# Kernel tuning notes

Measured on AMD Instinct MI355X. Metric: run time of the kernel, lower is better.

The kernel has to match this reference:

```python
import jax, jax.numpy as jnp
import numpy as np

N_NODES = 50000
N_EDGES = 800000
IN_C = 16
HID_C = 16
OUT_C = 10
N_GRAPHS = 500
EDGE_DIM = 3
MLP_HID = 25
BN_EPS = 1e-5


def setup_inputs() -> dict:
    key = jax.random.key(0)
    ks = iter(jax.random.split(key, 40))

    def nrm(shape, scale=1.0):
        return jax.random.normal(next(ks), shape, dtype=jnp.float32) * scale

    inp = {}
    inp["x"] = nrm((N_NODES, IN_C))
    inp["edge_index"] = jax.random.randint(next(ks), (2, N_EDGES), 0, N_NODES, dtype=jnp.int32)
    inp["edge_attr"] = jax.random.uniform(next(ks), (N_EDGES, EDGE_DIM), dtype=jnp.float32)
    inp["batch"] = jnp.sort(jax.random.randint(next(ks), (N_NODES,), 0, N_GRAPHS, dtype=jnp.int32))

    def bn_params():
        g = jax.random.uniform(next(ks), (MLP_HID,), minval=0.8, maxval=1.2, dtype=jnp.float32)
        b = nrm((MLP_HID,), 0.1)
        mu = nrm((MLP_HID,), 0.1)
        var = jax.random.uniform(next(ks), (MLP_HID,), minval=0.5, maxval=1.5, dtype=jnp.float32)
        return g, b, mu, var

    # edge MLP 1: 3 -> 25 -> IN_C*HID_C
    inp["W1a"] = nrm((EDGE_DIM, MLP_HID), 0.3)
    inp["b1a"] = nrm((MLP_HID,), 0.05)
    inp["g1"], inp["bt1"], inp["m1"], inp["v1"] = bn_params()
    inp["W1b"] = nrm((MLP_HID, IN_C * HID_C), 0.1)
    inp["b1b"] = nrm((IN_C * HID_C,), 0.05)
    inp["root1"] = nrm((IN_C, HID_C), 0.2)
    inp["bias1"] = nrm((HID_C,), 0.05)

    # edge MLP 2: 3 -> 25 -> HID_C*HID_C
    inp["W2a"] = nrm((EDGE_DIM, MLP_HID), 0.3)
    inp["b2a"] = nrm((MLP_HID,), 0.05)
    inp["g2"], inp["bt2"], inp["m2"], inp["v2"] = bn_params()
    inp["W2b"] = nrm((MLP_HID, HID_C * HID_C), 0.1)
    inp["b2b"] = nrm((HID_C * HID_C,), 0.05)
    inp["root2"] = nrm((HID_C, HID_C), 0.2)
    inp["bias2"] = nrm((HID_C,), 0.05)

    # final MLP([HID_C, OUT_C]) -> single plain linear (plain_last)
    inp["fcW"] = nrm((HID_C, OUT_C), 0.2)
    inp["fcb"] = nrm((OUT_C,), 0.05)
    return inp


def _edge_mlp(e, Wa, ba, g, bt, mu, var, Wb, bb):
    # Linear -> BatchNorm(eval) -> ReLU -> (dropout=eval identity) -> Linear
    h = e @ Wa + ba
    h = g * (h - mu) * jax.lax.rsqrt(var + BN_EPS) + bt
    h = jax.nn.relu(h)
    return h @ Wb + bb


def _nnconv(x, src, dst, w_edge, root, bias, out_dim):
    # message: x_j [E,in] times per-edge weight [E,in,out]
    msg = jnp.einsum("ei,eio->eo", x[src], w_edge)
    agg = jax.ops.segment_sum(msg, dst, num_segments=N_NODES)
    deg = jax.ops.segment_sum(jnp.ones((src.shape[0],), msg.dtype), dst, num_segments=N_NODES)
    agg = agg / jnp.maximum(deg, 1.0)[:, None]  # mean aggregation
    return agg + x @ root + bias


def reference(x, edge_index, edge_attr, batch,
              W1a, b1a, g1, bt1, m1, v1, W1b, b1b, root1, bias1,
              W2a, b2a, g2, bt2, m2, v2, W2b, b2b, root2, bias2,
              fcW, fcb):
    src, dst = edge_index[0], edge_index[1]

    w1 = _edge_mlp(edge_attr, W1a, b1a, g1, bt1, m1, v1, W1b, b1b).reshape(-1, IN_C, HID_C)
    x = jax.nn.elu(_nnconv(x, src, dst, w1, root1, bias1, HID_C))

    w2 = _edge_mlp(edge_attr, W2a, b2a, g2, bt2, m2, v2, W2b, b2b).reshape(-1, HID_C, HID_C)
    x = jax.nn.elu(_nnconv(x, src, dst, w2, root2, bias2, HID_C))

    # global mean pooling over graphs
    pooled = jax.ops.segment_sum(x, batch, num_segments=N_GRAPHS)
    cnt = jax.ops.segment_sum(jnp.ones((x.shape[0],), x.dtype), batch, num_segments=N_GRAPHS)
    pooled = pooled / jnp.maximum(cnt, 1.0)[:, None]

    return pooled @ fcW + fcb  # [N_GRAPHS, OUT_C]
```

## Files before the change

kernel.cpp:

```cpp
#include <hip/hip_runtime.h>
#include <math.h>

#define N_NODES 50000
#define N_EDGES 800000
#define IN_C 16
#define HID_C 16
#define OUT_C 10
#define N_GRAPHS 500
#define EDGE_DIM 3
#define MLP_HID 25
#define BN_EPS 1e-5f

#define SCAN_NB ((N_NODES + 255) / 256)

typedef __attribute__((ext_vector_type(8))) short short8;
typedef __attribute__((ext_vector_type(4))) float f32x4;
typedef __attribute__((ext_vector_type(2))) float f32x2;
union U4S8 { uint4 u; short8 s; };


__global__ __launch_bounds__(256) void prep_graph_kernel(
    const float* __restrict__ W1a, const float* __restrict__ b1a,
    const float* __restrict__ g1, const float* __restrict__ bt1,
    const float* __restrict__ m1, const float* __restrict__ v1,
    const float* __restrict__ W2a, const float* __restrict__ b2a,
    const float* __restrict__ g2, const float* __restrict__ bt2,
    const float* __restrict__ m2, const float* __restrict__ v2,
    const int* __restrict__ batch,
    float* __restrict__ AC1, float* __restrict__ AC2,
    int* __restrict__ goff)
{
    int t = threadIdx.x;
    if (blockIdx.x == 0) {
        if (t < 26) {
            int k = t;
            if (k < 25) {
                float sc = g1[k] / sqrtf(v1[k] + BN_EPS);
                AC1[k*4+0] = sc * W1a[0*MLP_HID+k];
                AC1[k*4+1] = sc * W1a[1*MLP_HID+k];
                AC1[k*4+2] = sc * W1a[2*MLP_HID+k];
                AC1[k*4+3] = sc * (b1a[k] - m1[k]) + bt1[k];
            } else {
                AC1[100] = 0.f; AC1[101] = 0.f; AC1[102] = 0.f; AC1[103] = 1.f;
            }
        } else if (t >= 32 && t < 58) {
            int k = t - 32;
            if (k < 25) {
                float sc = g2[k] / sqrtf(v2[k] + BN_EPS);
                AC2[k*4+0] = sc * W2a[0*MLP_HID+k];
                AC2[k*4+1] = sc * W2a[1*MLP_HID+k];
                AC2[k*4+2] = sc * W2a[2*MLP_HID+k];
                AC2[k*4+3] = sc * (b2a[k] - m2[k]) + bt2[k];
            } else {
                AC2[100] = 0.f; AC2[101] = 0.f; AC2[102] = 0.f; AC2[103] = 1.f;
            }
        }
    }
    int g = blockIdx.x * blockDim.x + t;
    if (g <= N_GRAPHS) {
        int lo = 0, hi = N_NODES;
        while (lo < hi) {
            int mid = (lo + hi) >> 1;
            if (batch[mid] < g) lo = mid + 1; else hi = mid;
        }
        goff[g] = lo;
    }
}

__global__ __launch_bounds__(256) void pack_w_kernel(
    const float* __restrict__ W1b, const float* __restrict__ b1b,
    const float* __restrict__ W2b, const float* __restrict__ b2b,
    unsigned int* __restrict__ WHI1, unsigned int* __restrict__ WHI2)
{
    int t = blockIdx.x * 256 + threadIdx.x;
    if (t >= 1664) return;
    const float *Wb, *bb; unsigned int *WH;
    int tl = t;
    if (t < 832) { Wb = W1b; bb = b1b; WH = WHI1; }
    else { tl = t - 832; Wb = W2b; bb = b2b; WH = WHI2; }
    int m = tl >> 6;
    int L = tl & 63;
    int q = L >> 4, o = L & 15;
    unsigned int hi[8];
    for (int j = 0; j < 8; ++j) {
        int kp = m*32 + q*8 + j;
        int k = kp >> 4, i = kp & 15;
        float w = (k < 25) ? Wb[k*256 + i*16 + o] : bb[i*16 + o];
        unsigned int u = __float_as_uint(w);
        hi[j] = (u + 0x7FFFu + ((u >> 16) & 1u)) >> 16;
    }
    int base = (m*64 + L) * 4;
    for (int d = 0; d < 4; ++d)
        WH[base + d] = hi[2*d] | (hi[2*d+1] << 16);
}


__global__ __launch_bounds__(256) void rank_kernel(const int* __restrict__ dst,
                                                   int* __restrict__ cnt,
                                                   int* __restrict__ rank) {
    int e = blockIdx.x * blockDim.x + threadIdx.x;
    if (e < N_EDGES) rank[e] = atomicAdd(&cnt[dst[e]], 1);
}

__global__ __launch_bounds__(256) void scan_p1(const int* __restrict__ cnt,
                                               int* __restrict__ bsum) {
    __shared__ int lds[256];
    int t = threadIdx.x;
    int idx = blockIdx.x * 256 + t;
    lds[t] = (idx < N_NODES) ? cnt[idx] : 0;
    __syncthreads();
    for (int d = 128; d > 0; d >>= 1) {
        if (t < d) lds[t] += lds[t + d];
        __syncthreads();
    }
    if (t == 0) bsum[blockIdx.x] = lds[0];
}

__global__ __launch_bounds__(256) void scan_p2(const int* __restrict__ bsum,
                                               int* __restrict__ bpre,
                                               int* __restrict__ off) {
    __shared__ int lds[256];
    int t = threadIdx.x;
    lds[t] = (t < SCAN_NB) ? bsum[t] : 0;
    __syncthreads();
    for (int d = 1; d < 256; d <<= 1) {
        int v = (t >= d) ? lds[t - d] : 0;
        __syncthreads();
        lds[t] += v;
        __syncthreads();
    }
    if (t < SCAN_NB) bpre[t] = (t > 0) ? lds[t - 1] : 0;
    if (t == 255) off[N_NODES] = lds[255];
}

__global__ __launch_bounds__(256) void scan_p3(const int* __restrict__ cnt,
                                               const int* __restrict__ bpre,
                                               int* __restrict__ off) {
    __shared__ int lds[256];
    int t = threadIdx.x;
    int idx = blockIdx.x * 256 + t;
    int v = (idx < N_NODES) ? cnt[idx] : 0;
    lds[t] = v;
    __syncthreads();
    for (int d = 1; d < 256; d <<= 1) {
        int u = (t >= d) ? lds[t - d] : 0;
        __syncthreads();
        lds[t] += u;
        __syncthreads();
    }
    if (idx < N_NODES) off[idx] = bpre[blockIdx.x] + lds[t] - v;
}

__global__ __launch_bounds__(256) void pos2_kernel(const int* __restrict__ dst,
                                                   const int* __restrict__ off,
                                                   int* __restrict__ rank) {
    int e = blockIdx.x * blockDim.x + threadIdx.x;
    if (e < N_EDGES) rank[e] = off[dst[e]] + rank[e];
}


__device__ __forceinline__ U4S8 packH(float h, float4 xl, float4 xh) {
    f32x2 h2; h2.x = h; h2.y = h;
    f32x2 m0; m0.x = xl.x; m0.y = xl.y; m0 *= h2;
    f32x2 m1; m1.x = xl.z; m1.y = xl.w; m1 *= h2;
    f32x2 m2; m2.x = xh.x; m2.y = xh.y; m2 *= h2;
    f32x2 m3; m3.x = xh.z; m3.y = xh.w; m3 *= h2;
    U4S8 r;
    r.u.x = __builtin_amdgcn_perm(__float_as_uint(m0.y), __float_as_uint(m0.x), 0x07060302u);
    r.u.y = __builtin_amdgcn_perm(__float_as_uint(m1.y), __float_as_uint(m1.x), 0x07060302u);
    r.u.z = __builtin_amdgcn_perm(__float_as_uint(m2.y), __float_as_uint(m2.x), 0x07060302u);
    r.u.w = __builtin_amdgcn_perm(__float_as_uint(m3.y), __float_as_uint(m3.x), 0x07060302u);
    return r;
}

__global__ __launch_bounds__(256) void edge_mfma3_kernel(
    const float* __restrict__ xin,
    const int* __restrict__ src,
    const int* __restrict__ P,
    const float* __restrict__ eattr,
    const float* __restrict__ AC,
    const unsigned int* __restrict__ WHI,
    float* __restrict__ msg_buf)
{
    const int tid  = threadIdx.x;
    const int wave = tid >> 6;
    const int lane = tid & 63;
    const int q    = lane >> 4;
    const int el   = lane & 15;
    const int i0   = (q & 1) * 8;
    const int b    = q >> 1;
    const int e0   = (blockIdx.x * 4 + wave) * 16;
    const int e    = e0 + el;

    const int s = src[e];
    const float a0 = eattr[(size_t)e*3+0];
    const float a1 = eattr[(size_t)e*3+1];
    const float a2 = eattr[(size_t)e*3+2];
    const uint4 pp = *(const uint4*)(P + e0 + q*4);
    const float4* xp = (const float4*)(xin + (size_t)s*16 + i0);
    const float4 xl = xp[0], xh = xp[1];

    f32x4 acc = {0.f, 0.f, 0.f, 0.f};
    #pragma unroll 1
    for (int m = 0; m < 13; ++m) {
        const float4 Ak = *(const float4*)(AC + (2*m + b)*4);
        U4S8 w; w.u = ((const uint4*)WHI)[m*64 + lane];
        float h = fmaxf(fmaf(a2, Ak.z, fmaf(a1, Ak.y, fmaf(a0, Ak.x, Ak.w))), 0.f);
        U4S8 hf = packH(h, xl, xh);
        acc = __builtin_amdgcn_mfma_f32_16x16x32_bf16(hf.s, w.s, acc, 0, 0, 0);
    }

    msg_buf[(size_t)((unsigned)pp.x) * HID_C + el] = acc[0];
    msg_buf[(size_t)((unsigned)pp.y) * HID_C + el] = acc[1];
    msg_buf[(size_t)((unsigned)pp.z) * HID_C + el] = acc[2];
    msg_buf[(size_t)((unsigned)pp.w) * HID_C + el] = acc[3];
}

__global__ __launch_bounds__(256) void node_gather_kernel(
    const float* __restrict__ xin, const float* __restrict__ msg_buf,
    const int* __restrict__ off,
    const float* __restrict__ root, const float* __restrict__ bias,
    float* __restrict__ xout)
{
    int t = blockIdx.x * blockDim.x + threadIdx.x;
    int n = t >> 4;
    int o = t & 15;
    if (n >= N_NODES) return;
    int lo = off[n], hi = off[n+1];
    float inv = 1.f / fmaxf((float)(hi - lo), 1.f);

    float s0 = 0.f, s1 = 0.f, s2 = 0.f, s3 = 0.f;
    int r = lo;
    for (; r + 4 <= hi; r += 4) {
        s0 += msg_buf[(size_t)r     * HID_C + o];
        s1 += msg_buf[(size_t)(r+1) * HID_C + o];
        s2 += msg_buf[(size_t)(r+2) * HID_C + o];
        s3 += msg_buf[(size_t)(r+3) * HID_C + o];
    }
    for (; r < hi; ++r) s0 += msg_buf[(size_t)r * HID_C + o];
    float s = (s0 + s1) + (s2 + s3);

    float acc = fmaf(s, inv, bias[o]);
    const float* xr = xin + (size_t)n * IN_C;
    #pragma unroll
    for (int i = 0; i < IN_C; ++i)
        acc = fmaf(xr[i], root[i*HID_C+o], acc);
    xout[(size_t)n*HID_C + o] = acc > 0.f ? acc : (expf(acc) - 1.f);
}

__global__ __launch_bounds__(64) void pool_final_kernel(
    const float* __restrict__ xin, const int* __restrict__ goff,
    const float* __restrict__ fcW, const float* __restrict__ fcb,
    float* __restrict__ out)
{
    __shared__ float part[4][HID_C];
    __shared__ float pooled[HID_C];
    int g = blockIdx.x;
    int t = threadIdx.x;
    int c = t & 15, sub = t >> 4;
    int lo = goff[g], hi = goff[g+1];
    float s = 0.f;
    for (int n = lo + sub; n < hi; n += 4)
        s += xin[(size_t)n*HID_C + c];
    part[sub][c] = s;
    __syncthreads();
    if (t < HID_C) {
        pooled[t] = (part[0][t] + part[1][t] + part[2][t] + part[3][t])
                    / fmaxf((float)(hi - lo), 1.f);
    }
    __syncthreads();
    if (t < OUT_C) {
        float acc = fcb[t];
        #pragma unroll
        for (int i = 0; i < HID_C; ++i)
            acc = fmaf(pooled[i], fcW[i*OUT_C+t], acc);
        out[g*OUT_C + t] = acc;
    }
}


extern "C" void kernel_launch(void* const* d_in, const int* in_sizes, int n_in,
                              void* d_out, int out_size, void* d_ws, size_t ws_size,
                              hipStream_t stream)
{
    const float* x     = (const float*)d_in[0];
    const int*   ei    = (const int*)d_in[1];
    const float* eattr = (const float*)d_in[2];
    const int*   batch = (const int*)d_in[3];
    const float* W1a   = (const float*)d_in[4];
    const float* b1a   = (const float*)d_in[5];
    const float* g1    = (const float*)d_in[6];
    const float* bt1   = (const float*)d_in[7];
    const float* m1    = (const float*)d_in[8];
    const float* v1    = (const float*)d_in[9];
    const float* W1b   = (const float*)d_in[10];
    const float* b1b   = (const float*)d_in[11];
    const float* root1 = (const float*)d_in[12];
    const float* bias1 = (const float*)d_in[13];
    const float* W2a   = (const float*)d_in[14];
    const float* b2a   = (const float*)d_in[15];
    const float* g2    = (const float*)d_in[16];
    const float* bt2   = (const float*)d_in[17];
    const float* m2    = (const float*)d_in[18];
    const float* v2    = (const float*)d_in[19];
    const float* W2b   = (const float*)d_in[20];
    const float* b2b   = (const float*)d_in[21];
    const float* root2 = (const float*)d_in[22];
    const float* bias2 = (const float*)d_in[23];
    const float* fcW   = (const float*)d_in[24];
    const float* fcb   = (const float*)d_in[25];

    const int* src = ei;
    const int* dst = ei + N_EDGES;

    float* ws   = (float*)d_ws;
    float* MSG  = ws;
    float* X1   = ws + 12800000;
    float* X2   = ws + 13600000;
    int*   RANK = (int*)(ws + 14400000);
    int*   CNT  = (int*)(ws + 15200000);
    int*   OFF  = (int*)(ws + 15250000);
    int*   GOFF = (int*)(ws + 15300064);
    unsigned int* WHI1 = (unsigned int*)(ws + 15300576);
    unsigned int* WHI2 = (unsigned int*)(ws + 15303904);
    float* AC1  = ws + 15307232;
    float* AC2  = ws + 15307344;
    int*   BSUM = (int*)(ws + 15307456);
    int*   BPRE = (int*)(ws + 15307712);

    hipMemsetAsync(CNT, 0, N_NODES * sizeof(int), stream);
    prep_graph_kernel<<<3, 256, 0, stream>>>(W1a, b1a, g1, bt1, m1, v1,
                                             W2a, b2a, g2, bt2, m2, v2,
                                             batch, AC1, AC2, GOFF);
    pack_w_kernel<<<7, 256, 0, stream>>>(W1b, b1b, W2b, b2b, WHI1, WHI2);
    rank_kernel<<<N_EDGES/256, 256, 0, stream>>>(dst, CNT, RANK);
    scan_p1<<<SCAN_NB, 256, 0, stream>>>(CNT, BSUM);
    scan_p2<<<1, 256, 0, stream>>>(BSUM, BPRE, OFF);
    scan_p3<<<SCAN_NB, 256, 0, stream>>>(CNT, BPRE, OFF);
    pos2_kernel<<<N_EDGES/256, 256, 0, stream>>>(dst, OFF, RANK);

    edge_mfma3_kernel<<<N_EDGES/64, 256, 0, stream>>>(x, src, RANK, eattr,
                                                      AC1, WHI1, MSG);
    node_gather_kernel<<<(N_NODES*16+255)/256, 256, 0, stream>>>(x, MSG, OFF,
                                                                 root1, bias1, X1);

    edge_mfma3_kernel<<<N_EDGES/64, 256, 0, stream>>>(X1, src, RANK, eattr,
                                                      AC2, WHI2, MSG);
    node_gather_kernel<<<(N_NODES*16+255)/256, 256, 0, stream>>>(X1, MSG, OFF,
                                                                 root2, bias2, X2);

    pool_final_kernel<<<N_GRAPHS, 64, 0, stream>>>(X2, GOFF, fcW, fcb, (float*)d_out);
}
```

Measured before the change: 310.4 us.

## Process two 16-edge tiles per wave in edge MFMA kernel and merge setup kernels

The edge kernel now has each wave handle 32 edges as two independent 16-edge MFMA chains. The per-iteration weight fragment and AC coefficient loads are shared across both chains, and the grid is halved. The two small setup kernels (weight packing and BN folding/graph offsets) are merged into one launch to save a kernel launch. Each lane now computes both even and odd hidden activations and selects one, which adds some VALU work and register pressure in exchange for reuse and more instruction-level parallelism.

```diff
diff --git a/kernel.cpp b/kernel.cpp
--- a/kernel.cpp
+++ b/kernel.cpp
@@ -19,21 +19,48 @@
 union U4S8 { uint4 u; short8 s; };
 
 
-__global__ __launch_bounds__(256) void prep_graph_kernel(
+__global__ __launch_bounds__(256) void setup_kernel(
     const float* __restrict__ W1a, const float* __restrict__ b1a,
     const float* __restrict__ g1, const float* __restrict__ bt1,
     const float* __restrict__ m1, const float* __restrict__ v1,
     const float* __restrict__ W2a, const float* __restrict__ b2a,
     const float* __restrict__ g2, const float* __restrict__ bt2,
     const float* __restrict__ m2, const float* __restrict__ v2,
+    const float* __restrict__ W1b, const float* __restrict__ b1b,
+    const float* __restrict__ W2b, const float* __restrict__ b2b,
     const int* __restrict__ batch,
     float* __restrict__ AC1, float* __restrict__ AC2,
+    unsigned int* __restrict__ WHI1, unsigned int* __restrict__ WHI2,
     int* __restrict__ goff)
 {
-    int t = threadIdx.x;
-    if (blockIdx.x == 0) {
-        if (t < 26) {
-            int k = t;
+    const int blk = blockIdx.x;
+    const int tid = threadIdx.x;
+    if (blk < 7) {
+        int t = blk * 256 + tid;
+        if (t >= 1664) return;
+        const float *Wb, *bb; unsigned int *WH;
+        int tl = t;
+        if (t < 832) { Wb = W1b; bb = b1b; WH = WHI1; }
+        else { tl = t - 832; Wb = W2b; bb = b2b; WH = WHI2; }
+        int m = tl >> 6;
+        int L = tl & 63;
+        int q = L >> 4, o = L & 15;
+        unsigned int hi[8];
+        for (int j = 0; j < 8; ++j) {
+            int kp = m*32 + q*8 + j;
+            int k = kp >> 4, i = kp & 15;
+            float w = (k < 25) ? Wb[k*256 + i*16 + o] : bb[i*16 + o];
+            unsigned int u = __float_as_uint(w);
+            hi[j] = (u + 0x7FFFu + ((u >> 16) & 1u)) >> 16;
+        }
+        int base = (m*64 + L) * 4;
+        for (int d = 0; d < 4; ++d)
+            WH[base + d] = hi[2*d] | (hi[2*d+1] << 16);
+        return;
+    }
+    if (blk == 7) {
+        if (tid < 26) {
+            int k = tid;
             if (k < 25) {
                 float sc = g1[k] / sqrtf(v1[k] + BN_EPS);
                 AC1[k*4+0] = sc * W1a[0*MLP_HID+k];
@@ -43,8 +70,8 @@
             } else {
                 AC1[100] = 0.f; AC1[101] = 0.f; AC1[102] = 0.f; AC1[103] = 1.f;
             }
-        } else if (t >= 32 && t < 58) {
-            int k = t - 32;
+        } else if (tid >= 32 && tid < 58) {
+            int k = tid - 32;
             if (k < 25) {
                 float sc = g2[k] / sqrtf(v2[k] + BN_EPS);
                 AC2[k*4+0] = sc * W2a[0*MLP_HID+k];
@@ -56,7 +83,7 @@
             }
         }
     }
-    int g = blockIdx.x * blockDim.x + t;
+    int g = (blk - 7) * 256 + tid;
     if (g <= N_GRAPHS) {
         int lo = 0, hi = N_NODES;
         while (lo < hi) {
@@ -65,33 +92,6 @@
         }
         goff[g] = lo;
     }
-}
-
-__global__ __launch_bounds__(256) void pack_w_kernel(
-    const float* __restrict__ W1b, const float* __restrict__ b1b,
-    const float* __restrict__ W2b, const float* __restrict__ b2b,
-    unsigned int* __restrict__ WHI1, unsigned int* __restrict__ WHI2)
-{
-    int t = blockIdx.x * 256 + threadIdx.x;
-    if (t >= 1664) return;
-    const float *Wb, *bb; unsigned int *WH;
-    int tl = t;
-    if (t < 832) { Wb = W1b; bb = b1b; WH = WHI1; }
-    else { tl = t - 832; Wb = W2b; bb = b2b; WH = WHI2; }
-    int m = tl >> 6;
-    int L = tl & 63;
-    int q = L >> 4, o = L & 15;
-    unsigned int hi[8];
-    for (int j = 0; j < 8; ++j) {
-        int kp = m*32 + q*8 + j;
-        int k = kp >> 4, i = kp & 15;
-        float w = (k < 25) ? Wb[k*256 + i*16 + o] : bb[i*16 + o];
-        unsigned int u = __float_as_uint(w);
-        hi[j] = (u + 0x7FFFu + ((u >> 16) & 1u)) >> 16;
-    }
-    int base = (m*64 + L) * 4;
-    for (int d = 0; d < 4; ++d)
-        WH[base + d] = hi[2*d] | (hi[2*d+1] << 16);
 }
 
 
@@ -173,7 +173,7 @@
     return r;
 }
 
-__global__ __launch_bounds__(256) void edge_mfma3_kernel(
+__global__ __launch_bounds__(256) void edge_mfma4_kernel(
     const float* __restrict__ xin,
     const int* __restrict__ src,
     const int* __restrict__ P,
@@ -188,32 +188,52 @@
     const int q    = lane >> 4;
     const int el   = lane & 15;
     const int i0   = (q & 1) * 8;
-    const int b    = q >> 1;
-    const int e0   = (blockIdx.x * 4 + wave) * 16;
-    const int e    = e0 + el;
-
-    const int s = src[e];
-    const float a0 = eattr[(size_t)e*3+0];
-    const float a1 = eattr[(size_t)e*3+1];
-    const float a2 = eattr[(size_t)e*3+2];
-    const uint4 pp = *(const uint4*)(P + e0 + q*4);
-    const float4* xp = (const float4*)(xin + (size_t)s*16 + i0);
-    const float4 xl = xp[0], xh = xp[1];
-
-    f32x4 acc = {0.f, 0.f, 0.f, 0.f};
+    const bool bsel = (q >> 1) != 0;
+    const int E0   = (blockIdx.x * 4 + wave) * 32;
+    const int eA   = E0 + el;
+    const int eB   = E0 + 16 + el;
+
+    const int sA = src[eA], sB = src[eB];
+    const float aA0 = eattr[(size_t)eA*3+0];
+    const float aA1 = eattr[(size_t)eA*3+1];
+    const float aA2 = eattr[(size_t)eA*3+2];
+    const float aB0 = eattr[(size_t)eB*3+0];
+    const float aB1 = eattr[(size_t)eB*3+1];
+    const float aB2 = eattr[(size_t)eB*3+2];
+    const uint4 ppA = *(const uint4*)(P + E0 + q*4);
+    const uint4 ppB = *(const uint4*)(P + E0 + 16 + q*4);
+    const float4* xpA = (const float4*)(xin + (size_t)sA*16 + i0);
+    const float4 xlA = xpA[0], xhA = xpA[1];
+    const float4* xpB = (const float4*)(xin + (size_t)sB*16 + i0);
+    const float4 xlB = xpB[0], xhB = xpB[1];
+
+    f32x4 accA = {0.f, 0.f, 0.f, 0.f};
+    f32x4 accB = {0.f, 0.f, 0.f, 0.f};
     #pragma unroll 1
     for (int m = 0; m < 13; ++m) {
-        const float4 Ak = *(const float4*)(AC + (2*m + b)*4);
+        const float4 Ae = *(const float4*)(AC + m*8);
+        const float4 Ao = *(const float4*)(AC + m*8 + 4);
         U4S8 w; w.u = ((const uint4*)WHI)[m*64 + lane];
-        float h = fmaxf(fmaf(a2, Ak.z, fmaf(a1, Ak.y, fmaf(a0, Ak.x, Ak.w))), 0.f);
-        U4S8 hf = packH(h, xl, xh);
-        acc = __builtin_amdgcn_mfma_f32_16x16x32_bf16(hf.s, w.s, acc, 0, 0, 0);
-    }
-
-    msg_buf[(size_t)((unsigned)pp.x) * HID_C + el] = acc[0];
-    msg_buf[(size_t)((unsigned)pp.y) * HID_C + el] = acc[1];
-    msg_buf[(size_t)((unsigned)pp.z) * HID_C + el] = acc[2];
-    msg_buf[(size_t)((unsigned)pp.w) * HID_C + el] = acc[3];
+        float hAe = fmaxf(fmaf(aA2, Ae.z, fmaf(aA1, Ae.y, fmaf(aA0, Ae.x, Ae.w))), 0.f);
+        float hAo = fmaxf(fmaf(aA2, Ao.z, fmaf(aA1, Ao.y, fmaf(aA0, Ao.x, Ao.w))), 0.f);
+        float hA  = bsel ? hAo : hAe;
+        float hBe = fmaxf(fmaf(aB2, Ae.z, fmaf(aB1, Ae.y, fmaf(aB0, Ae.x, Ae.w))), 0.f);
+        float hBo = fmaxf(fmaf(aB2, Ao.z, fmaf(aB1, Ao.y, fmaf(aB0, Ao.x, Ao.w))), 0.f);
+        float hB  = bsel ? hBo : hBe;
+        U4S8 hfA = packH(hA, xlA, xhA);
+        U4S8 hfB = packH(hB, xlB, xhB);
+        accA = __builtin_amdgcn_mfma_f32_16x16x32_bf16(hfA.s, w.s, accA, 0, 0, 0);
+        accB = __builtin_amdgcn_mfma_f32_16x16x32_bf16(hfB.s, w.s, accB, 0, 0, 0);
+    }
+
+    msg_buf[(size_t)((unsigned)ppA.x) * HID_C + el] = accA[0];
+    msg_buf[(size_t)((unsigned)ppA.y) * HID_C + el] = accA[1];
+    msg_buf[(size_t)((unsigned)ppA.z) * HID_C + el] = accA[2];
+    msg_buf[(size_t)((unsigned)ppA.w) * HID_C + el] = accA[3];
+    msg_buf[(size_t)((unsigned)ppB.x) * HID_C + el] = accB[0];
+    msg_buf[(size_t)((unsigned)ppB.y) * HID_C + el] = accB[1];
+    msg_buf[(size_t)((unsigned)ppB.z) * HID_C + el] = accB[2];
+    msg_buf[(size_t)((unsigned)ppB.w) * HID_C + el] = accB[3];
 }
 
 __global__ __launch_bounds__(256) void node_gather_kernel(
@@ -329,23 +349,23 @@
     int*   BPRE = (int*)(ws + 15307712);
 
     hipMemsetAsync(CNT, 0, N_NODES * sizeof(int), stream);
-    prep_graph_kernel<<<3, 256, 0, stream>>>(W1a, b1a, g1, bt1, m1, v1,
-                                             W2a, b2a, g2, bt2, m2, v2,
-                                             batch, AC1, AC2, GOFF);
-    pack_w_kernel<<<7, 256, 0, stream>>>(W1b, b1b, W2b, b2b, WHI1, WHI2);
+    setup_kernel<<<9, 256, 0, stream>>>(W1a, b1a, g1, bt1, m1, v1,
+                                        W2a, b2a, g2, bt2, m2, v2,
+                                        W1b, b1b, W2b, b2b, batch,
+                                        AC1, AC2, WHI1, WHI2, GOFF);
     rank_kernel<<<N_EDGES/256, 256, 0, stream>>>(dst, CNT, RANK);
     scan_p1<<<SCAN_NB, 256, 0, stream>>>(CNT, BSUM);
     scan_p2<<<1, 256, 0, stream>>>(BSUM, BPRE, OFF);
     scan_p3<<<SCAN_NB, 256, 0, stream>>>(CNT, BPRE, OFF);
     pos2_kernel<<<N_EDGES/256, 256, 0, stream>>>(dst, OFF, RANK);
 
-    edge_mfma3_kernel<<<N_EDGES/64, 256, 0, stream>>>(x, src, RANK, eattr,
-                                                      AC1, WHI1, MSG);
+    edge_mfma4_kernel<<<N_EDGES/128, 256, 0, stream>>>(x, src, RANK, eattr,
+                                                       AC1, WHI1, MSG);
     node_gather_kernel<<<(N_NODES*16+255)/256, 256, 0, stream>>>(x, MSG, OFF,
                                                                  root1, bias1, X1);
 
-    edge_mfma3_kernel<<<N_EDGES/64, 256, 0, stream>>>(X1, src, RANK, eattr,
-                                                      AC2, WHI2, MSG);
+    edge_mfma4_kernel<<<N_EDGES/128, 256, 0, stream>>>(X1, src, RANK, eattr,
+                                                       AC2, WHI2, MSG);
     node_gather_kernel<<<(N_NODES*16+255)/256, 256, 0, stream>>>(X1, MSG, OFF,
                                                                  root2, bias2, X2);
 
```

After: 277.7 us. 10.5% less time.
